# Kernel tuning notes

Hardware: AMD Instinct MI355X
Metric: run time of the kernel (lower is better)

Reference implementation:

```python
import jax, jax.numpy as jnp
import numpy as np
from jax import lax

# 4 directional difference kernels, stacked as OIHW [4,1,3,3]
# torch conv2d is cross-correlation; lax.conv_general_dilated with OIHW/NCHW matches.
_KERNELS = jnp.array([
    [[0, 0, 0], [-1, 1, 0], [0, 0, 0]],   # left:  x[i,j] - x[i,j-1]
    [[0, 0, 0], [0, 1, -1], [0, 0, 0]],   # right: x[i,j] - x[i,j+1]
    [[0, -1, 0], [0, 1, 0], [0, 0, 0]],   # up:    x[i,j] - x[i-1,j]
    [[0, 0, 0], [0, 1, 0], [0, -1, 0]],   # down:  x[i,j] - x[i+1,j]
], dtype=jnp.float32)[:, None, :, :]


def _avg_pool4(x):
    # x: [B,1,H,W] -> [B,1,H//4,W//4], non-overlapping 4x4 mean
    B, C, H, W = x.shape
    return x.reshape(B, C, H // 4, 4, W // 4, 4).mean(axis=(3, 5))


def _dir_diffs(x):
    # x: [B,1,h,w] -> [B,4,h,w]; zero-padded cross-correlation, padding=1
    return lax.conv_general_dilated(
        x, _KERNELS, window_strides=(1, 1), padding=((1, 1), (1, 1)),
        dimension_numbers=("NCHW", "OIHW", "NCHW"))


def setup_inputs() -> dict:
    key = jax.random.key(0)
    k1, k2 = jax.random.split(key)
    original = jax.random.uniform(k1, (32, 3, 512, 512), dtype=jnp.float32)
    enhanced = jax.random.uniform(k2, (32, 3, 512, 512), dtype=jnp.float32)
    return {"original": original, "enhanced": enhanced}


def reference(original, enhanced) -> jnp.ndarray:
    # channel mean, keepdim -> [B,1,H,W]
    o = jnp.mean(original, axis=1, keepdims=True)
    e = jnp.mean(enhanced, axis=1, keepdims=True)
    # 4x4 avg pool -> [B,1,H/4,W/4]
    op = _avg_pool4(o)
    ep = _avg_pool4(e)
    # 4 directional shift-diffs for both, squared differences summed over directions
    d = _dir_diffs(op) - _dir_diffs(ep)           # [B,4,h,w]
    loss = jnp.sum(d * d, axis=1, keepdims=True)  # [B,1,h,w]
    return loss
```

## Files before the change

### kernel.cpp

```cpp
#include <hip/hip_runtime.h>

#define HH 512
#define WW 512
#define PH 128
#define PW 128
#define CC 3

__global__ void __launch_bounds__(256)
pool_diff_kernel(const float* __restrict__ orig,
                 const float* __restrict__ enh,
                 float* __restrict__ g, int total) {
    int idx = blockIdx.x * blockDim.x + threadIdx.x;
    if (idx >= total) return;
    int j = idx & (PW - 1);
    int i = (idx >> 7) & (PH - 1);
    int b = idx >> 14;

    const size_t img = (size_t)HH * WW;
    const size_t base = (size_t)b * CC * img + (size_t)(i * 4) * WW + (size_t)(j * 4);

    float s = 0.0f;
#pragma unroll
    for (int c = 0; c < CC; ++c) {
#pragma unroll
        for (int r = 0; r < 4; ++r) {
            const size_t off = base + (size_t)c * img + (size_t)r * WW;
            const float4 o = *(const float4*)(orig + off);
            const float4 e = *(const float4*)(enh + off);
            s += (o.x - e.x) + (o.y - e.y) + (o.z - e.z) + (o.w - e.w);
        }
    }
    g[idx] = s * (1.0f / 48.0f);
}

__global__ void __launch_bounds__(256)
stencil_loss_kernel(const float* __restrict__ g,
                    float* __restrict__ out, int total) {
    int idx = blockIdx.x * blockDim.x + threadIdx.x;
    if (idx >= total) return;
    int j = idx & (PW - 1);
    int i = (idx >> 7) & (PH - 1);

    float c = g[idx];
    float l = (j > 0)      ? g[idx - 1]  : 0.0f;
    float r = (j < PW - 1) ? g[idx + 1]  : 0.0f;
    float u = (i > 0)      ? g[idx - PW] : 0.0f;
    float d = (i < PH - 1) ? g[idx + PW] : 0.0f;

    float dl = c - l, dr = c - r, du = c - u, dd = c - d;
    out[idx] = dl * dl + dr * dr + du * du + dd * dd;
}

extern "C" void kernel_launch(void* const* d_in, const int* in_sizes, int n_in,
                              void* d_out, int out_size, void* d_ws, size_t ws_size,
                              hipStream_t stream) {
    const float* orig = (const float*)d_in[0];
    const float* enh  = (const float*)d_in[1];
    float* out = (float*)d_out;
    float* g   = (float*)d_ws;

    const int batch = in_sizes[0] / (CC * HH * WW);
    const int total = batch * PH * PW;

    const int block = 256;
    const int grid = (total + block - 1) / block;

    pool_diff_kernel<<<grid, block, 0, stream>>>(orig, enh, g, total);
    stencil_loss_kernel<<<grid, block, 0, stream>>>(g, out, total);
}
```

Before: 213.0 us.

## Split each pooled row across two thread halves with shared-memory combine

The pooling kernel now gives each block one pooled output row. The two 128-thread halves each read two of the four input rows and their partial sums are combined through shared memory. This doubles the thread count and the number of waves, which gives more memory-level parallelism and fewer loads per thread. The cost is a __syncthreads and half the threads sitting idle during the final write.

Measured after the change: 211.1 us. No clear change (-0.9%).

```diff
diff --git a/kernel.cpp b/kernel.cpp
--- a/kernel.cpp
+++ b/kernel.cpp
@@ -9,28 +9,35 @@
 __global__ void __launch_bounds__(256)
 pool_diff_kernel(const float* __restrict__ orig,
                  const float* __restrict__ enh,
-                 float* __restrict__ g, int total) {
-    int idx = blockIdx.x * blockDim.x + threadIdx.x;
-    if (idx >= total) return;
-    int j = idx & (PW - 1);
-    int i = (idx >> 7) & (PH - 1);
-    int b = idx >> 14;
+                 float* __restrict__ g) {
+    const int bi   = blockIdx.x;
+    const int tid  = threadIdx.x;
+    const int j    = tid & (PW - 1);
+    const int half = tid >> 7;
 
-    const size_t img = (size_t)HH * WW;
-    const size_t base = (size_t)b * CC * img + (size_t)(i * 4) * WW + (size_t)(j * 4);
+    const size_t img     = (size_t)HH * WW;
+    const int    b       = bi >> 7;
+    const int    i       = bi & (PH - 1);
+    const size_t rowbase = (size_t)b * CC * img + (size_t)(4 * i) * WW;
 
     float s = 0.0f;
 #pragma unroll
     for (int c = 0; c < CC; ++c) {
-#pragma unroll
-        for (int r = 0; r < 4; ++r) {
-            const size_t off = base + (size_t)c * img + (size_t)r * WW;
-            const float4 o = *(const float4*)(orig + off);
-            const float4 e = *(const float4*)(enh + off);
-            s += (o.x - e.x) + (o.y - e.y) + (o.z - e.z) + (o.w - e.w);
-        }
+        const size_t off = rowbase + (size_t)c * img + (size_t)(2 * half) * WW + (size_t)(4 * j);
+        const float4 o0 = *(const float4*)(orig + off);
+        const float4 o1 = *(const float4*)(orig + off + WW);
+        const float4 e0 = *(const float4*)(enh + off);
+        const float4 e1 = *(const float4*)(enh + off + WW);
+        s += (o0.x - e0.x) + (o0.y - e0.y) + (o0.z - e0.z) + (o0.w - e0.w)
+           + (o1.x - e1.x) + (o1.y - e1.y) + (o1.z - e1.z) + (o1.w - e1.w);
     }
-    g[idx] = s * (1.0f / 48.0f);
+
+    __shared__ float part[2][PW];
+    part[half][j] = s;
+    __syncthreads();
+    if (tid < PW) {
+        g[(size_t)bi * PW + tid] = (part[0][tid] + part[1][tid]) * (1.0f / 48.0f);
+    }
 }
 
 __global__ void __launch_bounds__(256)
@@ -62,9 +69,9 @@
     const int batch = in_sizes[0] / (CC * HH * WW);
     const int total = batch * PH * PW;
 
+    pool_diff_kernel<<<batch * PH, 256, 0, stream>>>(orig, enh, g);
+
     const int block = 256;
     const int grid = (total + block - 1) / block;
-
-    pool_diff_kernel<<<grid, block, 0, stream>>>(orig, enh, g, total);
     stencil_loss_kernel<<<grid, block, 0, stream>>>(g, out, total);
 }
```

## Assign one wavefront per pooled row strip with batched vector loads

Applied to the files above, without the earlier changes.

Restructures the pooling kernel so each 64-lane wavefront handles a full pooled row, with each lane computing two output columns. All 16 float4 loads per channel are issued before any arithmetic, raising outstanding memory requests per thread. A launch-bounds occupancy hint is added. The larger register footprint may limit occupancy or cause spills.

Result: no change. 213.4 us (+0.2%).

```diff
diff --git a/kernel.cpp b/kernel.cpp
--- a/kernel.cpp
+++ b/kernel.cpp
@@ -6,31 +6,46 @@
 #define PW 128
 #define CC 3
 
-__global__ void __launch_bounds__(256)
+__global__ void __launch_bounds__(256, 4)
 pool_diff_kernel(const float* __restrict__ orig,
                  const float* __restrict__ enh,
-                 float* __restrict__ g, int total) {
-    int idx = blockIdx.x * blockDim.x + threadIdx.x;
-    if (idx >= total) return;
-    int j = idx & (PW - 1);
-    int i = (idx >> 7) & (PH - 1);
-    int b = idx >> 14;
+                 float* __restrict__ g) {
+    const int wid  = blockIdx.x * 4 + (threadIdx.x >> 6);
+    const int lane = threadIdx.x & 63;
 
-    const size_t img = (size_t)HH * WW;
-    const size_t base = (size_t)b * CC * img + (size_t)(i * 4) * WW + (size_t)(j * 4);
+    const int b = wid >> 7;
+    const int i = wid & (PH - 1);
 
-    float s = 0.0f;
+    const size_t img  = (size_t)HH * WW;
+    const size_t base = (size_t)b * CC * img + (size_t)(4 * i) * WW;
+
+    float s0 = 0.0f, s1 = 0.0f;
+
 #pragma unroll
     for (int c = 0; c < CC; ++c) {
+        const size_t cb = base + (size_t)c * img + (size_t)lane * 4;
+        float4 ov[8], ev[8];
 #pragma unroll
-        for (int r = 0; r < 4; ++r) {
-            const size_t off = base + (size_t)c * img + (size_t)r * WW;
-            const float4 o = *(const float4*)(orig + off);
-            const float4 e = *(const float4*)(enh + off);
-            s += (o.x - e.x) + (o.y - e.y) + (o.z - e.z) + (o.w - e.w);
+        for (int t = 0; t < 8; ++t) {
+            const int r = t >> 1, h = t & 1;
+            ov[t] = *(const float4*)(orig + cb + (size_t)r * WW + (size_t)h * 256);
+        }
+#pragma unroll
+        for (int t = 0; t < 8; ++t) {
+            const int r = t >> 1, h = t & 1;
+            ev[t] = *(const float4*)(enh + cb + (size_t)r * WW + (size_t)h * 256);
+        }
+#pragma unroll
+        for (int t = 0; t < 8; ++t) {
+            const float d = (ov[t].x - ev[t].x) + (ov[t].y - ev[t].y)
+                          + (ov[t].z - ev[t].z) + (ov[t].w - ev[t].w);
+            if ((t & 1) == 0) s0 += d; else s1 += d;
         }
     }
-    g[idx] = s * (1.0f / 48.0f);
+
+    float* grow = g + (size_t)wid * PW;
+    grow[lane]      = s0 * (1.0f / 48.0f);
+    grow[lane + 64] = s1 * (1.0f / 48.0f);
 }
 
 __global__ void __launch_bounds__(256)
@@ -59,12 +74,13 @@
     float* out = (float*)d_out;
     float* g   = (float*)d_ws;
 
-    const int batch = in_sizes[0] / (CC * HH * WW);
-    const int total = batch * PH * PW;
+    const int batch  = in_sizes[0] / (CC * HH * WW);
+    const int strips = batch * PH;
+    const int total  = batch * PH * PW;
+
+    pool_diff_kernel<<<strips / 4, 256, 0, stream>>>(orig, enh, g);
 
     const int block = 256;
     const int grid = (total + block - 1) / block;
-
-    pool_diff_kernel<<<grid, block, 0, stream>>>(orig, enh, g, total);
     stencil_loss_kernel<<<grid, block, 0, stream>>>(g, out, total);
 }
```

## Stage pooling input strips into LDS via async global_load_lds

Applied to the files above, without the earlier changes.

Reworks the pooling kernel so each block handles one 4-row strip across all channels. It copies the strip into shared memory with asynchronous global-to-LDS loads that are fully coalesced, then has 128 threads reduce from LDS. The goal is better coalescing and fewer outstanding VGPR loads on a purely bandwidth-bound read. The cost is 48KB of LDS per block, which limits occupancy, and half the threads sit idle during the reduction.

Result: no change. 210.0 us (-1.4%).

```diff
diff --git a/kernel.cpp b/kernel.cpp
--- a/kernel.cpp
+++ b/kernel.cpp
@@ -5,32 +5,53 @@
 #define PH 128
 #define PW 128
 #define CC 3
+#define STRIP_FLOATS (CC * 4 * WW)
+
+__device__ __forceinline__ void async_cp16(const float* gsrc, float* ldst) {
+    __builtin_amdgcn_global_load_lds(
+        (const __attribute__((address_space(1))) void*)gsrc,
+        (__attribute__((address_space(3))) void*)ldst,
+        16, 0, 0);
+}
 
 __global__ void __launch_bounds__(256)
 pool_diff_kernel(const float* __restrict__ orig,
                  const float* __restrict__ enh,
-                 float* __restrict__ g, int total) {
-    int idx = blockIdx.x * blockDim.x + threadIdx.x;
-    if (idx >= total) return;
-    int j = idx & (PW - 1);
-    int i = (idx >> 7) & (PH - 1);
-    int b = idx >> 14;
+                 float* __restrict__ g) {
+    __shared__ __align__(16) float so[STRIP_FLOATS];
+    __shared__ __align__(16) float se[STRIP_FLOATS];
 
-    const size_t img = (size_t)HH * WW;
-    const size_t base = (size_t)b * CC * img + (size_t)(i * 4) * WW + (size_t)(j * 4);
+    const int strip = blockIdx.x;
+    const int wave  = threadIdx.x >> 6;
+    const int lane  = threadIdx.x & 63;
 
-    float s = 0.0f;
+    const int b = strip >> 7;
+    const int i = strip & (PH - 1);
+    const size_t img  = (size_t)HH * WW;
+    const size_t base = (size_t)b * CC * img + (size_t)(4 * i) * WW;
+
 #pragma unroll
-    for (int c = 0; c < CC; ++c) {
+    for (int t = 0; t < 6; ++t) {
+        const int k = wave * 6 + t;
+        const int c = k >> 3;
+        const int q = k & 7;
+        const size_t goff = base + (size_t)c * img + (size_t)q * 256 + (size_t)lane * 4;
+        async_cp16(orig + goff, so + k * 256);
+        async_cp16(enh  + goff, se + k * 256);
+    }
+    __syncthreads();
+
+    if (threadIdx.x < PW) {
+        const int j = threadIdx.x;
+        float s = 0.0f;
 #pragma unroll
-        for (int r = 0; r < 4; ++r) {
-            const size_t off = base + (size_t)c * img + (size_t)r * WW;
-            const float4 o = *(const float4*)(orig + off);
-            const float4 e = *(const float4*)(enh + off);
-            s += (o.x - e.x) + (o.y - e.y) + (o.z - e.z) + (o.w - e.w);
+        for (int row = 0; row < 12; ++row) {
+            const float4 o4 = *(const float4*)(so + row * WW + 4 * j);
+            const float4 e4 = *(const float4*)(se + row * WW + 4 * j);
+            s += (o4.x - e4.x) + (o4.y - e4.y) + (o4.z - e4.z) + (o4.w - e4.w);
         }
+        g[(size_t)strip * PW + j] = s * (1.0f / 48.0f);
     }
-    g[idx] = s * (1.0f / 48.0f);
 }
 
 __global__ void __launch_bounds__(256)
@@ -59,12 +80,13 @@
     float* out = (float*)d_out;
     float* g   = (float*)d_ws;
 
-    const int batch = in_sizes[0] / (CC * HH * WW);
-    const int total = batch * PH * PW;
+    const int batch  = in_sizes[0] / (CC * HH * WW);
+    const int strips = batch * PH;
+    const int total  = batch * PH * PW;
+
+    pool_diff_kernel<<<strips, 256, 0, stream>>>(orig, enh, g);
 
     const int block = 256;
     const int grid = (total + block - 1) / block;
-
-    pool_diff_kernel<<<grid, block, 0, stream>>>(orig, enh, g, total);
     stencil_loss_kernel<<<grid, block, 0, stream>>>(g, out, total);
 }
```
